# Kernel tuning notes

Hardware: AMD Instinct MI355X
Metric: run time of the kernel (lower is better)

## Reference

```python
import jax, jax.numpy as jnp
import numpy as np

B, S, D = 2, 2048, 1024
H, DH = 16, 64  # num_heads, hidden_dimension (per-head)


def setup_inputs() -> dict:
    key = jax.random.key(0)
    ks = jax.random.split(key, 9)
    s = 1.0 / np.sqrt(D)
    so = 1.0 / np.sqrt(H * DH)
    return {
        "x": jax.random.normal(ks[0], (B, S, D), dtype=jnp.float32),
        "Wq": jax.random.uniform(ks[1], (D, H * DH), jnp.float32, -s, s),
        "bq": jax.random.uniform(ks[2], (H * DH,), jnp.float32, -s, s),
        "Wk": jax.random.uniform(ks[3], (D, H * DH), jnp.float32, -s, s),
        "bk": jax.random.uniform(ks[4], (H * DH,), jnp.float32, -s, s),
        "Wv": jax.random.uniform(ks[5], (D, H * DH), jnp.float32, -s, s),
        "bv": jax.random.uniform(ks[6], (H * DH,), jnp.float32, -s, s),
        "Wo": jax.random.uniform(ks[7], (H * DH, D), jnp.float32, -so, so),
        "bo": jax.random.uniform(ks[8], (D,), jnp.float32, -so, so),
    }


def reference(x, Wq, bq, Wk, bk, Wv, bv, Wo, bo):
    b, s, _ = x.shape
    # project and split heads: [b, h, s, dh]
    q = (x @ Wq + bq).reshape(b, s, H, DH).transpose(0, 2, 1, 3)
    k = (x @ Wk + bk).reshape(b, s, H, DH).transpose(0, 2, 1, 3)
    v = (x @ Wv + bv).reshape(b, s, H, DH).transpose(0, 2, 1, 3)
    scores = jnp.einsum('bhqd,bhkd->bhqk', q, k) / jnp.sqrt(jnp.float32(DH))
    causal = jnp.triu(jnp.ones((s, s), dtype=bool), k=1)
    scores = jnp.where(causal, -jnp.inf, scores)
    weights = jax.nn.softmax(scores, axis=-1)
    out = jnp.einsum('bhqk,bhkd->bhqd', weights, v)
    out = out.transpose(0, 2, 1, 3).reshape(b, s, H * DH)
    return out @ Wo + bo
```

## Files before the change

kernel.cpp:

```cpp
#include <hip/hip_runtime.h>

#define B_  2
#define S_  2048
#define D_  1024
#define H_  16
#define DH_ 64
#define NDH (H_*DH_)
#define BS_ (B_*S_)
#define PER ((size_t)B_*H_*S_*DH_)

typedef __bf16 bf16;
typedef bf16 bf16x8 __attribute__((ext_vector_type(8)));
typedef bf16 bf16x4 __attribute__((ext_vector_type(4)));
typedef float f32x4 __attribute__((ext_vector_type(4)));

#define QSCALE 0.18033688011112042f

#define AS1 __attribute__((address_space(1)))
#define AS3 __attribute__((address_space(3)))
__device__ inline void gld16(const bf16* g, bf16* l) {
    __builtin_amdgcn_global_load_lds((const AS1 void*)g, (AS3 void*)l, 16, 0, 0);
}

__global__ __launch_bounds__(256) void prep(
        const float* __restrict__ x,
        const float* __restrict__ W0, const float* __restrict__ W1,
        const float* __restrict__ W2, const float* __restrict__ W3,
        bf16* __restrict__ xb, bf16* __restrict__ T0, bf16* __restrict__ T1,
        bf16* __restrict__ T2, bf16* __restrict__ T3) {
    __shared__ float T[32][33];
    int bid = blockIdx.x, t = threadIdx.x;
    if (bid < 4096) {
        int i = (bid * 256 + t) * 4;
        float4 v = *(const float4*)(x + i);
        bf16x4 o = { (bf16)v.x, (bf16)v.y, (bf16)v.z, (bf16)v.w };
        *(bf16x4*)(xb + i) = o;
        return;
    }
    int r2 = bid - 4096;
    int z = r2 >> 10, w = r2 & 1023;
    const float* W = (z == 0) ? W0 : (z == 1) ? W1 : (z == 2) ? W2 : W3;
    bf16* Wt = (z == 0) ? T0 : (z == 1) ? T1 : (z == 2) ? T2 : T3;
    int k0 = (w >> 5) * 32, n0 = (w & 31) * 32;
    int r = t >> 3, c = (t & 7) * 4;
    float4 v = *(const float4*)(W + (size_t)(k0 + r) * 1024 + n0 + c);
    T[c + 0][r] = v.x; T[c + 1][r] = v.y; T[c + 2][r] = v.z; T[c + 3][r] = v.w;
    __syncthreads();
    bf16x4 o = { (bf16)T[r][c], (bf16)T[r][c + 1], (bf16)T[r][c + 2], (bf16)T[r][c + 3] };
    *(bf16x4*)(Wt + (size_t)(n0 + r) * 1024 + k0 + c) = o;
}

__global__ __launch_bounds__(256) void qkv_gemm(
        const bf16* __restrict__ A, const bf16* __restrict__ Bt,
        const float* __restrict__ bq, const float* __restrict__ bk,
        const float* __restrict__ bv, bf16* __restrict__ Qout, bf16* __restrict__ Vt) {
    __shared__ __align__(16) bf16 As[3][128 * 32];
    __shared__ __align__(16) bf16 Bs[3][128 * 32];
    int tid = threadIdx.x, wave = tid >> 6, lane = tid & 63;
    int quad = lane >> 4, l16 = lane & 15;

    int flat = blockIdx.y * 24 + blockIdx.x;
    int swz  = (flat & 7) * 96 + (flat >> 3);
    int bm = (swz / 24) * 128, bn = (swz % 24) * 128;
    int wm = (wave >> 1) * 64, wn = (wave & 1) * 64;

    int sr = lane >> 2;
    int sc = (((lane & 3) ^ ((sr ^ (sr >> 2)) & 3)) * 8);
    const bf16* Ag0 = A + (size_t)(bm + (wave * 2 + 0) * 16 + sr) * 1024 + sc;
    const bf16* Ag1 = A + (size_t)(bm + (wave * 2 + 1) * 16 + sr) * 1024 + sc;
    const bf16* Bg0 = Bt + (size_t)(bn + (wave * 2 + 0) * 16 + sr) * 1024 + sc;
    const bf16* Bg1 = Bt + (size_t)(bn + (wave * 2 + 1) * 16 + sr) * 1024 + sc;
    int la0 = (wave * 2 + 0) * 512;
    int la1 = (wave * 2 + 1) * 512;

    int cs0 = ((0 ^ ((l16 ^ (l16 >> 2)) & 3)) ^ quad) * 8;
    int rsw = (l16 ^ (l16 >> 2)) & 3;

    f32x4 acc[4][4] = {};

    auto stage = [&](int buf, int t) {
        int k0 = t * 32;
        gld16(Ag0 + k0, &As[buf][la0]);
        gld16(Ag1 + k0, &As[buf][la1]);
        gld16(Bg0 + k0, &Bs[buf][la0]);
        gld16(Bg1 + k0, &Bs[buf][la1]);
    };
    (void)cs0;

    stage(0, 0);
    stage(1, 1);

    for (int t = 0; t < 32; ++t) {
        if (t < 30) asm volatile("s_waitcnt vmcnt(4)" ::: "memory");
        else        asm volatile("s_waitcnt vmcnt(0)" ::: "memory");
        __builtin_amdgcn_s_barrier();
        if (t + 2 < 32) stage((t + 2) % 3, t + 2);
        int cur = t % 3;
        bf16x8 af[4], bfr[4];
        #pragma unroll
        for (int i = 0; i < 4; ++i)
            af[i] = *(const bf16x8*)&As[cur][(wm + i * 16 + l16) * 32 + ((0 ^ quad ^ rsw)) * 8];
        #pragma unroll
        for (int j = 0; j < 4; ++j)
            bfr[j] = *(const bf16x8*)&Bs[cur][(wn + j * 16 + l16) * 32 + ((0 ^ quad ^ rsw)) * 8];
        #pragma unroll
        for (int i = 0; i < 4; ++i)
          #pragma unroll
          for (int j = 0; j < 4; ++j)
            acc[i][j] = __builtin_amdgcn_mfma_f32_16x16x32_bf16(af[i], bfr[j], acc[i][j], 0, 0, 0);
    }
    __builtin_amdgcn_s_barrier();

    #pragma unroll
    for (int i = 0; i < 4; ++i)
      #pragma unroll
      for (int j = 0; j < 4; ++j) {
        int col = bn + wn + j * 16 + l16;
        float bias = (col < 1024) ? bq[col] : (col < 2048) ? bk[col - 1024] : bv[col - 2048];
        int qkv = col >> 10, cw = col & 1023;
        int hh = cw >> 6, d = cw & 63;
        int row0 = bm + wm + i * 16 + quad * 4;
        int bb = row0 >> 11, s0 = row0 & 2047;
        if (qkv < 2) {
            float scl = (qkv == 0) ? QSCALE : 1.0f;
            #pragma unroll
            for (int r = 0; r < 4; ++r)
                Qout[(size_t)qkv * PER + (((size_t)bb * H_ + hh) * S_ + s0 + r) * DH_ + d] =
                    (bf16)((acc[i][j][r] + bias) * scl);
        } else {
            bf16x4 pack;
            #pragma unroll
            for (int r = 0; r < 4; ++r) pack[r] = (bf16)(acc[i][j][r] + bias);
            *(bf16x4*)&Vt[(((size_t)bb * H_ + hh) * DH_ + d) * S_ + s0] = pack;
        }
      }
}

__global__ __launch_bounds__(256) void gemm_proj(
        const bf16* __restrict__ A, const bf16* __restrict__ Bt,
        const float* __restrict__ bias, float* __restrict__ out) {
    __shared__ __align__(16) bf16 As[3][128 * 32];
    __shared__ __align__(16) bf16 Bs[3][64 * 32];
    int tid = threadIdx.x, wave = tid >> 6, lane = tid & 63;
    int quad = lane >> 4, l16 = lane & 15;

    int flat = blockIdx.y * 16 + blockIdx.x;
    int swz  = (flat & 7) * 64 + (flat >> 3);
    int bm = (swz / 16) * 128, bn = (swz % 16) * 64;
    int wm = (wave >> 1) * 64, wn = (wave & 1) * 32;

    int sr = lane >> 2;
    int sc = (((lane & 3) ^ ((sr ^ (sr >> 2)) & 3)) * 8);
    const bf16* Ag0 = A + (size_t)(bm + (wave * 2 + 0) * 16 + sr) * 1024 + sc;
    const bf16* Ag1 = A + (size_t)(bm + (wave * 2 + 1) * 16 + sr) * 1024 + sc;
    const bf16* Bg0 = Bt + (size_t)(bn + wave * 16 + sr) * 1024 + sc;
    int la0 = (wave * 2 + 0) * 512;
    int la1 = (wave * 2 + 1) * 512;
    int lb0 = wave * 512;

    int rsw = (l16 ^ (l16 >> 2)) & 3;

    f32x4 acc[4][2] = {};

    auto stage = [&](int buf, int t) {
        int k0 = t * 32;
        gld16(Ag0 + k0, &As[buf][la0]);
        gld16(Ag1 + k0, &As[buf][la1]);
        gld16(Bg0 + k0, &Bs[buf][lb0]);
    };

    stage(0, 0);
    stage(1, 1);

    for (int t = 0; t < 32; ++t) {
        if (t < 30) asm volatile("s_waitcnt vmcnt(3)" ::: "memory");
        else        asm volatile("s_waitcnt vmcnt(0)" ::: "memory");
        __builtin_amdgcn_s_barrier();
        if (t + 2 < 32) stage((t + 2) % 3, t + 2);
        int cur = t % 3;
        bf16x8 af[4], bfr[2];
        #pragma unroll
        for (int i = 0; i < 4; ++i)
            af[i] = *(const bf16x8*)&As[cur][(wm + i * 16 + l16) * 32 + (quad ^ rsw) * 8];
        #pragma unroll
        for (int j = 0; j < 2; ++j)
            bfr[j] = *(const bf16x8*)&Bs[cur][(wn + j * 16 + l16) * 32 + (quad ^ rsw) * 8];
        #pragma unroll
        for (int i = 0; i < 4; ++i)
          #pragma unroll
          for (int j = 0; j < 2; ++j)
            acc[i][j] = __builtin_amdgcn_mfma_f32_16x16x32_bf16(af[i], bfr[j], acc[i][j], 0, 0, 0);
    }
    __builtin_amdgcn_s_barrier();

    #pragma unroll
    for (int i = 0; i < 4; ++i)
      #pragma unroll
      for (int j = 0; j < 2; ++j) {
        int col = bn + wn + j * 16 + l16;
        float b = bias[col];
        #pragma unroll
        for (int r = 0; r < 4; ++r) {
            int row = bm + wm + i * 16 + quad * 4 + r;
            out[(size_t)row * 1024 + col] = acc[i][j][r] + b;
        }
      }
}

__global__ __launch_bounds__(256) void flash10(
        const bf16* __restrict__ Q, const bf16* __restrict__ K,
        const bf16* __restrict__ Vt, bf16* __restrict__ O) {
    int bh = blockIdx.x;
    int b = bh >> 4, h = bh & 15;
    int t = 31 - blockIdx.y;
    int q0 = t * 64;
    int nkt = t + 1;
    int tid = threadIdx.x;
    int wave = tid >> 6, lane = tid & 63;
    int quad = lane >> 4, l16 = lane & 15;
    int lm = l16 & 7;

    __shared__ __align__(16) bf16 Kl[2][64 * 64];
    __shared__ __align__(16) bf16 Vl[2][64 * 64];
    __shared__ bf16 P[4][16][72];

    const bf16* Qb = Q + (size_t)bh * S_ * DH_;
    const bf16* Kb = K + (size_t)bh * S_ * DH_;
    const bf16* Vb = Vt + (size_t)bh * DH_ * S_;

    bf16x8 qf[2];
    {
        const bf16* qp = Qb + (size_t)(q0 + wave * 16 + l16) * DH_ + quad * 8;
        qf[0] = *(const bf16x8*)(qp);
        qf[1] = *(const bf16x8*)(qp + 32);
    }

    bf16x8 ones;
    #pragma unroll
    for (int j = 0; j < 8; ++j) ones[j] = (l16 == 0) ? (bf16)1.0f : (bf16)0.0f;

    f32x4 oacc[4] = {};
    f32x4 lacc = {};

    int r8 = lane >> 3, c8 = lane & 7;
    int sco = ((c8 ^ r8) * 8);

    auto stage = [&](int buf, int kt) {
        int kv0 = kt * 64;
        #pragma unroll
        for (int g = 0; g < 2; ++g) {
            int row = wave * 16 + g * 8;
            gld16(Kb + (size_t)(kv0 + row + r8) * DH_ + sco, &Kl[buf][row * 64]);
            gld16(Vb + (size_t)(row + r8) * S_ + kv0 + sco,   &Vl[buf][row * 64]);
        }
    };

    stage(0, 0);
    __syncthreads();

    for (int kt = 0; kt < nkt; ++kt) {
        int buf = kt & 1;
        if (kt + 1 < nkt) stage(buf ^ 1, kt + 1);
        int kv0 = kt * 64;

        bf16x8 kf[4][2];
        #pragma unroll
        for (int ns = 0; ns < 4; ++ns) {
            int row = ns * 16 + l16;
            kf[ns][0] = *(const bf16x8*)&Kl[buf][row * 64 + ((quad)     ^ lm) * 8];
            kf[ns][1] = *(const bf16x8*)&Kl[buf][row * 64 + ((4 + quad) ^ lm) * 8];
        }

        f32x4 sacc[4] = {};
        #pragma unroll
        for (int ns = 0; ns < 4; ++ns) {
            sacc[ns] = __builtin_amdgcn_mfma_f32_16x16x32_bf16(qf[0], kf[ns][0], sacc[ns], 0, 0, 0);
            sacc[ns] = __builtin_amdgcn_mfma_f32_16x16x32_bf16(qf[1], kf[ns][1], sacc[ns], 0, 0, 0);
        }

        bool diag = (kt == nkt - 1);
        #pragma unroll
        for (int ns = 0; ns < 4; ++ns)
          #pragma unroll
          for (int r = 0; r < 4; ++r) {
              float p = __builtin_amdgcn_exp2f(sacc[ns][r]);
              if (diag) {
                  int kv = kv0 + ns * 16 + l16;
                  int qq = q0 + wave * 16 + quad * 4 + r;
                  if (kv > qq) p = 0.f;
              }
              P[wave][quad * 4 + r][ns * 16 + l16] = (bf16)p;
          }

        #pragma unroll
        for (int ks = 0; ks < 2; ++ks) {
            bf16x8 pf = *(const bf16x8*)&P[wave][l16][ks * 32 + quad * 8];
            lacc = __builtin_amdgcn_mfma_f32_16x16x32_bf16(pf, ones, lacc, 0, 0, 0);
            #pragma unroll
            for (int ds = 0; ds < 4; ++ds) {
                bf16x8 vf = *(const bf16x8*)&Vl[buf][(ds * 16 + l16) * 64 + ((ks * 4 + quad) ^ lm) * 8];
                oacc[ds] = __builtin_amdgcn_mfma_f32_16x16x32_bf16(pf, vf, oacc[ds], 0, 0, 0);
            }
        }

        __syncthreads();
    }

    float ls[4];
    #pragma unroll
    for (int r = 0; r < 4; ++r) ls[r] = __shfl(lacc[r], quad << 4);
    #pragma unroll
    for (int ds = 0; ds < 4; ++ds)
      #pragma unroll
      for (int r = 0; r < 4; ++r) {
          int qq = q0 + wave * 16 + quad * 4 + r;
          O[((size_t)b * S_ + qq) * NDH + h * DH_ + ds * 16 + l16] = (bf16)(oacc[ds][r] / ls[r]);
      }
}

extern "C" void kernel_launch(void* const* d_in, const int* in_sizes, int n_in,
                              void* d_out, int out_size, void* d_ws, size_t ws_size,
                              hipStream_t stream) {
    const float* x  = (const float*)d_in[0];
    const float* Wq = (const float*)d_in[1];
    const float* bq = (const float*)d_in[2];
    const float* Wk = (const float*)d_in[3];
    const float* bk = (const float*)d_in[4];
    const float* Wv = (const float*)d_in[5];
    const float* bv = (const float*)d_in[6];
    const float* Wo = (const float*)d_in[7];
    const float* bo = (const float*)d_in[8];
    float* out = (float*)d_out;

    bf16* ws = (bf16*)d_ws;
    const size_t M1 = (size_t)1024 * 1024;
    bf16* xb    = ws;
    bf16* WqkvT = ws + 4 * M1;
    bf16* WoT   = ws + 7 * M1;
    bf16* Qw    = ws + 8 * M1;
    bf16* Vtw   = ws + 16 * M1;
    bf16* Ow    = ws + 20 * M1;

    prep<<<8192, 256, 0, stream>>>(x, Wq, Wk, Wv, Wo,
                                   xb, WqkvT, WqkvT + M1, WqkvT + 2 * M1, WoT);

    qkv_gemm<<<dim3(3072 / 128, BS_ / 128), 256, 0, stream>>>(xb, WqkvT, bq, bk, bv, Qw, Vtw);

    flash10<<<dim3(B_ * H_, 32), 256, 0, stream>>>(Qw, Qw + PER, Vtw, Ow);

    gemm_proj<<<dim3(1024 / 64, BS_ / 128), 256, 0, stream>>>(Ow, WoT, bo, out);
}
```

Baseline: 182.7 us.

## Double flash attention query tile to 128 rows per block for K/V reuse

The attention kernel now gives each block 128 query rows, with each wave handling two 16-row sub-tiles, instead of 64 rows. Every K/V tile staged into shared memory is then reused for twice as many queries, which halves K/V global traffic and barrier count per query row. In exchange the grid is half as large (512 blocks), there are more registers per wave, and the causal mask is applied on the last two KV tiles. Some of those masked tiles are wasted work for the first query sub-tiles.

Result: slower. 200.1 us (+9.6%).

```diff
diff --git a/kernel.cpp b/kernel.cpp
--- a/kernel.cpp
+++ b/kernel.cpp
@@ -73,7 +73,6 @@
     int la0 = (wave * 2 + 0) * 512;
     int la1 = (wave * 2 + 1) * 512;
 
-    int cs0 = ((0 ^ ((l16 ^ (l16 >> 2)) & 3)) ^ quad) * 8;
     int rsw = (l16 ^ (l16 >> 2)) & 3;
 
     f32x4 acc[4][4] = {};
@@ -85,7 +84,6 @@
         gld16(Bg0 + k0, &Bs[buf][la0]);
         gld16(Bg1 + k0, &Bs[buf][la1]);
     };
-    (void)cs0;
 
     stage(0, 0);
     stage(1, 1);
@@ -99,10 +97,10 @@
         bf16x8 af[4], bfr[4];
         #pragma unroll
         for (int i = 0; i < 4; ++i)
-            af[i] = *(const bf16x8*)&As[cur][(wm + i * 16 + l16) * 32 + ((0 ^ quad ^ rsw)) * 8];
+            af[i] = *(const bf16x8*)&As[cur][(wm + i * 16 + l16) * 32 + (quad ^ rsw) * 8];
         #pragma unroll
         for (int j = 0; j < 4; ++j)
-            bfr[j] = *(const bf16x8*)&Bs[cur][(wn + j * 16 + l16) * 32 + ((0 ^ quad ^ rsw)) * 8];
+            bfr[j] = *(const bf16x8*)&Bs[cur][(wn + j * 16 + l16) * 32 + (quad ^ rsw) * 8];
         #pragma unroll
         for (int i = 0; i < 4; ++i)
           #pragma unroll
@@ -207,14 +205,14 @@
       }
 }
 
-__global__ __launch_bounds__(256) void flash10(
+__global__ __launch_bounds__(256) void flash11(
         const bf16* __restrict__ Q, const bf16* __restrict__ K,
         const bf16* __restrict__ Vt, bf16* __restrict__ O) {
     int bh = blockIdx.x;
     int b = bh >> 4, h = bh & 15;
-    int t = 31 - blockIdx.y;
-    int q0 = t * 64;
-    int nkt = t + 1;
+    int t = 15 - blockIdx.y;
+    int q0 = t * 128;
+    int nkt = 2 * t + 2;
     int tid = threadIdx.x;
     int wave = tid >> 6, lane = tid & 63;
     int quad = lane >> 4, l16 = lane & 15;
@@ -222,25 +220,26 @@
 
     __shared__ __align__(16) bf16 Kl[2][64 * 64];
     __shared__ __align__(16) bf16 Vl[2][64 * 64];
-    __shared__ bf16 P[4][16][72];
+    __shared__ bf16 P[4][2][16][72];
 
     const bf16* Qb = Q + (size_t)bh * S_ * DH_;
     const bf16* Kb = K + (size_t)bh * S_ * DH_;
     const bf16* Vb = Vt + (size_t)bh * DH_ * S_;
 
-    bf16x8 qf[2];
-    {
-        const bf16* qp = Qb + (size_t)(q0 + wave * 16 + l16) * DH_ + quad * 8;
-        qf[0] = *(const bf16x8*)(qp);
-        qf[1] = *(const bf16x8*)(qp + 32);
+    bf16x8 qf[2][2];
+    #pragma unroll
+    for (int s = 0; s < 2; ++s) {
+        const bf16* qp = Qb + (size_t)(q0 + wave * 32 + s * 16 + l16) * DH_ + quad * 8;
+        qf[s][0] = *(const bf16x8*)(qp);
+        qf[s][1] = *(const bf16x8*)(qp + 32);
     }
 
     bf16x8 ones;
     #pragma unroll
     for (int j = 0; j < 8; ++j) ones[j] = (l16 == 0) ? (bf16)1.0f : (bf16)0.0f;
 
-    f32x4 oacc[4] = {};
-    f32x4 lacc = {};
+    f32x4 oacc[2][4] = {};
+    f32x4 lacc[2] = {};
 
     int r8 = lane >> 3, c8 = lane & 7;
     int sco = ((c8 ^ r8) * 8);
@@ -271,51 +270,61 @@
             kf[ns][1] = *(const bf16x8*)&Kl[buf][row * 64 + ((4 + quad) ^ lm) * 8];
         }
 
-        f32x4 sacc[4] = {};
-        #pragma unroll
-        for (int ns = 0; ns < 4; ++ns) {
-            sacc[ns] = __builtin_amdgcn_mfma_f32_16x16x32_bf16(qf[0], kf[ns][0], sacc[ns], 0, 0, 0);
-            sacc[ns] = __builtin_amdgcn_mfma_f32_16x16x32_bf16(qf[1], kf[ns][1], sacc[ns], 0, 0, 0);
-        }
-
-        bool diag = (kt == nkt - 1);
-        #pragma unroll
-        for (int ns = 0; ns < 4; ++ns)
-          #pragma unroll
-          for (int r = 0; r < 4; ++r) {
-              float p = __builtin_amdgcn_exp2f(sacc[ns][r]);
-              if (diag) {
-                  int kv = kv0 + ns * 16 + l16;
-                  int qq = q0 + wave * 16 + quad * 4 + r;
-                  if (kv > qq) p = 0.f;
-              }
-              P[wave][quad * 4 + r][ns * 16 + l16] = (bf16)p;
+        f32x4 sacc[2][4] = {};
+        #pragma unroll
+        for (int s = 0; s < 2; ++s)
+          #pragma unroll
+          for (int ns = 0; ns < 4; ++ns) {
+            sacc[s][ns] = __builtin_amdgcn_mfma_f32_16x16x32_bf16(qf[s][0], kf[ns][0], sacc[s][ns], 0, 0, 0);
+            sacc[s][ns] = __builtin_amdgcn_mfma_f32_16x16x32_bf16(qf[s][1], kf[ns][1], sacc[s][ns], 0, 0, 0);
           }
 
+        bool diag = (kt >= nkt - 2);
+        #pragma unroll
+        for (int s = 0; s < 2; ++s)
+          #pragma unroll
+          for (int ns = 0; ns < 4; ++ns)
+            #pragma unroll
+            for (int r = 0; r < 4; ++r) {
+                float p = __builtin_amdgcn_exp2f(sacc[s][ns][r]);
+                if (diag) {
+                    int kv = kv0 + ns * 16 + l16;
+                    int qq = q0 + wave * 32 + s * 16 + quad * 4 + r;
+                    if (kv > qq) p = 0.f;
+                }
+                P[wave][s][quad * 4 + r][ns * 16 + l16] = (bf16)p;
+            }
+
         #pragma unroll
         for (int ks = 0; ks < 2; ++ks) {
-            bf16x8 pf = *(const bf16x8*)&P[wave][l16][ks * 32 + quad * 8];
-            lacc = __builtin_amdgcn_mfma_f32_16x16x32_bf16(pf, ones, lacc, 0, 0, 0);
+            bf16x8 pf0 = *(const bf16x8*)&P[wave][0][l16][ks * 32 + quad * 8];
+            bf16x8 pf1 = *(const bf16x8*)&P[wave][1][l16][ks * 32 + quad * 8];
+            lacc[0] = __builtin_amdgcn_mfma_f32_16x16x32_bf16(pf0, ones, lacc[0], 0, 0, 0);
+            lacc[1] = __builtin_amdgcn_mfma_f32_16x16x32_bf16(pf1, ones, lacc[1], 0, 0, 0);
             #pragma unroll
             for (int ds = 0; ds < 4; ++ds) {
                 bf16x8 vf = *(const bf16x8*)&Vl[buf][(ds * 16 + l16) * 64 + ((ks * 4 + quad) ^ lm) * 8];
-                oacc[ds] = __builtin_amdgcn_mfma_f32_16x16x32_bf16(pf, vf, oacc[ds], 0, 0, 0);
+                oacc[0][ds] = __builtin_amdgcn_mfma_f32_16x16x32_bf16(pf0, vf, oacc[0][ds], 0, 0, 0);
+                oacc[1][ds] = __builtin_amdgcn_mfma_f32_16x16x32_bf16(pf1, vf, oacc[1][ds], 0, 0, 0);
             }
         }
 
         __syncthreads();
     }
 
-    float ls[4];
-    #pragma unroll
-    for (int r = 0; r < 4; ++r) ls[r] = __shfl(lacc[r], quad << 4);
-    #pragma unroll
-    for (int ds = 0; ds < 4; ++ds)
-      #pragma unroll
-      for (int r = 0; r < 4; ++r) {
-          int qq = q0 + wave * 16 + quad * 4 + r;
-          O[((size_t)b * S_ + qq) * NDH + h * DH_ + ds * 16 + l16] = (bf16)(oacc[ds][r] / ls[r]);
-      }
+    #pragma unroll
+    for (int s = 0; s < 2; ++s) {
+        float ls[4];
+        #pragma unroll
+        for (int r = 0; r < 4; ++r) ls[r] = __shfl(lacc[s][r], quad << 4);
+        #pragma unroll
+        for (int ds = 0; ds < 4; ++ds)
+          #pragma unroll
+          for (int r = 0; r < 4; ++r) {
+              int qq = q0 + wave * 32 + s * 16 + quad * 4 + r;
+              O[((size_t)b * S_ + qq) * NDH + h * DH_ + ds * 16 + l16] = (bf16)(oacc[s][ds][r] / ls[r]);
+          }
+    }
 }
 
 extern "C" void kernel_launch(void* const* d_in, const int* in_sizes, int n_in,
@@ -346,7 +355,7 @@
 
     qkv_gemm<<<dim3(3072 / 128, BS_ / 128), 256, 0, stream>>>(xb, WqkvT, bq, bk, bv, Qw, Vtw);
 
-    flash10<<<dim3(B_ * H_, 32), 256, 0, stream>>>(Qw, Qw + PER, Vtw, Ow);
+    flash11<<<dim3(B_ * H_, 16), 256, 0, stream>>>(Qw, Qw + PER, Vtw, Ow);
 
     gemm_proj<<<dim3(1024 / 64, BS_ / 128), 256, 0, stream>>>(Ow, WoT, bo, out);
 }
```
